# Optimization experiments

Measured on AMD Instinct MI355X. Metric: run time of the kernel, lower is better.

Reference implementation:

```python
import jax, jax.numpy as jnp
import numpy as np

B, N, D, H, L = 2, 2048, 128, 8, 3
V = 32          # NUM_ATOM_TYPES (assumed)
DH = D // H
SCALE = 1.0 / (DH ** 0.5)
NEG = -1e9      # stands in for -inf in the additive attention mask
EPS = 1e-5


def _ln(x, g, b):
    m = x.mean(-1, keepdims=True)
    v = ((x - m) ** 2).mean(-1, keepdims=True)
    return (x - m) / jnp.sqrt(v + EPS) * g + b


def setup_inputs() -> dict:
    key = jax.random.key(0)
    ks = jax.random.split(key, 24)
    nrm = lambda k, shape, std=0.02: jax.random.normal(k, shape, jnp.float32) * std
    atom_embed = nrm(ks[0], (V, D)).at[0].set(0.0)  # padding_idx = 0
    cons_embed = nrm(ks[1], (1, 1, D))
    in_w = nrm(ks[2], (D, D)); in_b = jnp.zeros((D,), jnp.float32)
    qkv_w = nrm(ks[3], (L, 3 * D, D)); qkv_b = jnp.zeros((L, 3 * D), jnp.float32)
    out_w = nrm(ks[4], (L, D, D)); out_b = jnp.zeros((L, D), jnp.float32)
    ln1_g = jnp.ones((L, D), jnp.float32); ln1_b = jnp.zeros((L, D), jnp.float32)
    ln2_g = jnp.ones((L, D), jnp.float32); ln2_b = jnp.zeros((L, D), jnp.float32)
    ff1_w = nrm(ks[5], (L, 4 * D, D)); ff1_b = jnp.zeros((L, 4 * D), jnp.float32)
    ff2_w = nrm(ks[6], (L, D, 4 * D)); ff2_b = jnp.zeros((L, D), jnp.float32)
    struct_bias = nrm(ks[7], (L,), 0.5)  # scalar per layer (init 0 in torch; randomized to exercise the path)
    head_ln_g = jnp.ones((D,), jnp.float32); head_ln_b = jnp.zeros((D,), jnp.float32)
    head_w = nrm(ks[8], (1, D)); head_b = jnp.zeros((1,), jnp.float32)
    is_atom = jax.random.bernoulli(ks[9], 0.5, (B, N))
    atom_id = jax.random.randint(ks[10], (B, N), 0, V)
    mask = jax.random.bernoulli(ks[11], 0.9, (B, N))
    adjacency = (jax.random.uniform(ks[12], (B, N, N)) < 0.002).astype(jnp.float32)
    adjacency = jnp.maximum(adjacency, jnp.eye(N, dtype=jnp.float32)[None])  # self-loops
    root_idx = jax.random.randint(ks[13], (B,), 0, N)
    return dict(atom_embed=atom_embed, cons_embed=cons_embed, in_w=in_w, in_b=in_b,
                qkv_w=qkv_w, qkv_b=qkv_b, out_w=out_w, out_b=out_b,
                ln1_g=ln1_g, ln1_b=ln1_b, ln2_g=ln2_g, ln2_b=ln2_b,
                ff1_w=ff1_w, ff1_b=ff1_b, ff2_w=ff2_w, ff2_b=ff2_b,
                struct_bias=struct_bias, head_ln_g=head_ln_g, head_ln_b=head_ln_b,
                head_w=head_w, head_b=head_b, adjacency=adjacency,
                is_atom=is_atom, atom_id=atom_id, mask=mask, root_idx=root_idx)


def reference(atom_embed, cons_embed, in_w, in_b, qkv_w, qkv_b, out_w, out_b,
              ln1_g, ln1_b, ln2_g, ln2_b, ff1_w, ff1_b, ff2_w, ff2_b,
              struct_bias, head_ln_g, head_ln_b, head_w, head_b,
              adjacency, is_atom, atom_id, mask, root_idx):
    # node embeddings
    ae = atom_embed[jnp.clip(atom_id, 0, V - 1)]                     # [B,N,D]
    h = jnp.where(is_atom[..., None], ae, jnp.broadcast_to(cons_embed, (B, N, D)))
    h = h @ in_w.T + in_b
    # additive attention mask: valid pairs OK; invalid query rows attend only to self
    pair_ok = mask[:, :, None] & mask[:, None, :]
    eye = jnp.eye(N, dtype=bool)[None]
    ok = pair_ok | ((~mask)[:, :, None] & eye)
    am = jnp.where(ok, 0.0, NEG).astype(jnp.float32)                 # [B,N,N]
    for i in range(L):
        x = _ln(h, ln1_g[i], ln1_b[i])
        qkv = (x @ qkv_w[i].T + qkv_b[i]).reshape(B, N, 3, H, DH)
        q, k, v = (jnp.transpose(qkv[:, :, j], (0, 2, 1, 3)) for j in range(3))  # [B,H,N,DH]
        scores = jnp.einsum('bhqd,bhkd->bhqk', q, k) * SCALE \
                 + struct_bias[i] * adjacency[:, None] + am[:, None]
        attn = jax.nn.softmax(scores, axis=-1)
        o = jnp.einsum('bhqk,bhkd->bhqd', attn, v)
        o = jnp.transpose(o, (0, 2, 1, 3)).reshape(B, N, D)
        h = h + (o @ out_w[i].T + out_b[i])
        x2 = _ln(h, ln2_g[i], ln2_b[i])
        f = jax.nn.gelu(x2 @ ff1_w[i].T + ff1_b[i], approximate=False)
        h = h + (f @ ff2_w[i].T + ff2_b[i])
    pooled = h[jnp.arange(B), root_idx]                              # [B,D]
    p = _ln(pooled, head_ln_g, head_ln_b)
    return (p @ head_w.T + head_b)[:, 0]                             # [B]
```

## Files before the change

kernel.cpp:

```cpp
#include <hip/hip_runtime.h>
#include <cmath>

#define NB 2
#define NN 2048
#define ND 128
#define NH 8
#define NL 3
#define NV 32
#define NDH 16
#define LN_EPS 1e-5f
#define QSCALE 0.36067376022224085f

typedef __bf16 bf8_t __attribute__((ext_vector_type(8)));
typedef __bf16 bf4_t __attribute__((ext_vector_type(4)));
typedef float f4x __attribute__((ext_vector_type(4)));
typedef float f16x __attribute__((ext_vector_type(16)));

struct CastArgs {
  const float* s[5];
  __bf16* d[5];
  int startblk[5];
};
__global__ __launch_bounds__(256) void castall_kernel(CastArgs a) {
  int blk = blockIdx.x;
  int seg = 0;
#pragma unroll
  for (int i = 1; i < 5; i++) seg += (blk >= a.startblk[i]) ? 1 : 0;
  int i4 = (blk - a.startblk[seg]) * 256 + threadIdx.x;
  float4 v = ((const float4*)a.s[seg])[i4];
  bf4_t p = {(__bf16)v.x, (__bf16)v.y, (__bf16)v.z, (__bf16)v.w};
  ((bf4_t*)a.d[seg])[i4] = p;
}

__global__ __launch_bounds__(256) void adjbits_kernel(const float* __restrict__ adj,
                                                      unsigned long long* __restrict__ bits) {
  int g = (blockIdx.x * 4 + (threadIdx.x >> 6)) * 4;
  int lane = threadIdx.x & 63;
  const float* p = adj + (size_t)g * 64 + lane;
  unsigned long long w0 = __ballot(p[0] != 0.0f);
  unsigned long long w1 = __ballot(p[64] != 0.0f);
  unsigned long long w2 = __ballot(p[128] != 0.0f);
  unsigned long long w3 = __ballot(p[192] != 0.0f);
  if (lane == 0) {
    bits[g] = w0; bits[g + 1] = w1; bits[g + 2] = w2; bits[g + 3] = w3;
  }
}

__global__ void maskbits_kernel(const int* __restrict__ mask,
                                unsigned long long* __restrict__ bits) {
  int g = blockIdx.x * 4 + (threadIdx.x >> 6);
  int lane = threadIdx.x & 63;
  int v = mask[g * 64 + lane];
  unsigned long long bal = __ballot(v != 0);
  if (lane == 0) bits[g] = bal;
}

template <int IN, int OUT2>
__global__ __launch_bounds__(512) void fused_kernel(
    const __bf16* __restrict__ Xb,
    const float* __restrict__ atom_embed, const float* __restrict__ cons_embed,
    const int* __restrict__ is_atom, const int* __restrict__ atom_id,
    const __bf16* __restrict__ W1, const float* __restrict__ b1,
    float* __restrict__ H,
    const float* __restrict__ lng, const float* __restrict__ lnb,
    const __bf16* __restrict__ W2, const float* __restrict__ b2,
    __bf16* __restrict__ Fb,
    __bf16* __restrict__ Qb, __bf16* __restrict__ Kb, __bf16* __restrict__ Vt) {
  constexpr int K1 = (IN == 2) ? 512 : 128;
  constexpr int XD = K1 + 16;
  __shared__ __bf16 Xs[16][XD];
  __shared__ __bf16 Ws[128][136];
  __shared__ float Hs[16][132];
  __shared__ __bf16 X2[16][136];
  int m0 = blockIdx.x * 16;
  int t = threadIdx.x;
  int lane = t & 63, w = t >> 6;
  int l15 = lane & 15, quad = lane >> 4;

  if constexpr (IN == 0) {
    int r = t >> 5, c = t & 31;
    int row = m0 + r;
    int id = atom_id[row];
    id = id < 0 ? 0 : (id > NV - 1 ? NV - 1 : id);
    const float* src = is_atom[row] ? (atom_embed + (size_t)id * ND) : cons_embed;
    float4 v = *(const float4*)&src[c * 4];
    bf4_t p = {(__bf16)v.x, (__bf16)v.y, (__bf16)v.z, (__bf16)v.w};
    *(bf4_t*)&Xs[r][c * 4] = p;
  } else if constexpr (IN == 1) {
    int r = t >> 5, c = t & 31;
    *(bf4_t*)&Xs[r][c * 4] = *(const bf4_t*)&Xb[(size_t)(m0 + r) * 128 + c * 4];
  } else {
#pragma unroll
    for (int c = t; c < 1024; c += 512) {
      int r = c >> 6, ch = c & 63;
      *(bf8_t*)&Xs[r][ch * 8] = *(const bf8_t*)&Xb[(size_t)(m0 + r) * 512 + ch * 8];
    }
  }

  f4x acc = {0.f, 0.f, 0.f, 0.f};
  for (int kc = 0; kc < K1 / 128; kc++) {
    if (kc) __syncthreads();
#pragma unroll
    for (int c = t; c < 2048; c += 512) {
      int r = c >> 4, ch = c & 15;
      *(bf8_t*)&Ws[r][ch * 8] = *(const bf8_t*)&W1[(size_t)r * K1 + kc * 128 + ch * 8];
    }
    __syncthreads();
#pragma unroll
    for (int kk = 0; kk < 4; kk++) {
      bf8_t a = *(const bf8_t*)&Xs[l15][kc * 128 + kk * 32 + quad * 8];
      bf8_t b = *(const bf8_t*)&Ws[w * 16 + l15][kk * 32 + quad * 8];
      acc = __builtin_amdgcn_mfma_f32_16x16x32_bf16(a, b, acc, 0, 0, 0);
    }
  }
  {
    int n = w * 16 + l15;
    float bv = b1[n];
#pragma unroll
    for (int r = 0; r < 4; r++) {
      int m = quad * 4 + r;
      float v = acc[r] + bv;
      if constexpr (IN != 0) v += H[(size_t)(m0 + m) * ND + n];
      H[(size_t)(m0 + m) * ND + n] = v;
      Hs[m][n] = v;
    }
  }
  __syncthreads();

  if constexpr (OUT2 != 0) {
    {
      int r = t >> 5, c = t & 31;
      float4 v = *(const float4*)&Hs[r][c * 4];
      float s1 = v.x + v.y + v.z + v.w;
      float s2 = v.x * v.x + v.y * v.y + v.z * v.z + v.w * v.w;
#pragma unroll
      for (int m = 16; m >= 1; m >>= 1) {
        s1 += __shfl_xor(s1, m, 64);
        s2 += __shfl_xor(s2, m, 64);
      }
      float mean = s1 * (1.0f / ND);
      float var = s2 * (1.0f / ND) - mean * mean;
      float rstd = rsqrtf(var + LN_EPS);
      float4 gg = *(const float4*)&lng[c * 4];
      float4 bb = *(const float4*)&lnb[c * 4];
      bf4_t p;
      p[0] = (__bf16)((v.x - mean) * rstd * gg.x + bb.x);
      p[1] = (__bf16)((v.y - mean) * rstd * gg.y + bb.y);
      p[2] = (__bf16)((v.z - mean) * rstd * gg.z + bb.z);
      p[3] = (__bf16)((v.w - mean) * rstd * gg.w + bb.w);
      *(bf4_t*)&X2[r][c * 4] = p;
    }
    __syncthreads();

    constexpr int NCH = (OUT2 == 1) ? 4 : 3;
#pragma unroll
    for (int nc = 0; nc < NCH; nc++) {
#pragma unroll
      for (int c = t; c < 2048; c += 512) {
        int r = c >> 4, ch = c & 15;
        *(bf8_t*)&Ws[r][ch * 8] = *(const bf8_t*)&W2[(size_t)(nc * 128 + r) * 128 + ch * 8];
      }
      __syncthreads();
      f4x a2 = {0.f, 0.f, 0.f, 0.f};
#pragma unroll
      for (int kk = 0; kk < 4; kk++) {
        bf8_t a = *(const bf8_t*)&X2[l15][kk * 32 + quad * 8];
        bf8_t b = *(const bf8_t*)&Ws[w * 16 + l15][kk * 32 + quad * 8];
        a2 = __builtin_amdgcn_mfma_f32_16x16x32_bf16(a, b, a2, 0, 0, 0);
      }
      int n = nc * 128 + w * 16 + l15;
      float bv = b2[n];
#pragma unroll
      for (int r = 0; r < 4; r++) {
        int m = m0 + quad * 4 + r;
        float v = a2[r] + bv;
        if constexpr (OUT2 == 1) {
          v = 0.5f * v * (1.0f + erff(v * 0.70710678118f));
          Fb[(size_t)m * 512 + n] = (__bf16)v;
        } else {
          if (nc == 0) Qb[(size_t)m * ND + n] = (__bf16)(v * QSCALE);
          else if (nc == 1) Kb[(size_t)m * ND + n - ND] = (__bf16)v;
          else {
            int c2 = n - 2 * ND, hh = c2 >> 4, d0 = c2 & 15;
            int bb = m >> 11, nn = m & 2047;
            Vt[((size_t)((bb * NH + hh) * NDH + d0)) * NN + nn] = (__bf16)v;
          }
        }
      }
      __syncthreads();
    }
  }
}

__global__ __launch_bounds__(512) void attn_kernel(
    const __bf16* __restrict__ Qb, const __bf16* __restrict__ Kb,
    const __bf16* __restrict__ Vt, const unsigned int* __restrict__ adjbits,
    const unsigned int* __restrict__ maskbits, const int* __restrict__ mask,
    const float* __restrict__ sbias, int layer, __bf16* __restrict__ o) {
  int b = blockIdx.z, hh = blockIdx.y, q0 = blockIdx.x * 32;
  int wave = threadIdx.x >> 6;
  int lane = threadIdx.x & 63;
  int l31 = lane & 31, hi = lane >> 5;
  int l15 = lane & 15, quad = lane >> 4;
  float esb = __expf(sbias[layer]);
  const int bN = b * NN;
  const int kw0 = wave * 256;

  __shared__ __bf16 Pbuf[8][32][40];
  __shared__ float Ored[8][32][17];
  __shared__ float Lred[8][32];

  bf8_t Qf = *(const bf8_t*)(Qb + (size_t)(bN + q0 + l31) * ND + hh * NDH + hi * 8);

  int q = q0 + l31;
  int mq = mask[bN + q];
  const unsigned int* adjp = adjbits + (size_t)(bN + q) * (NN / 32) + (kw0 >> 5);
  const unsigned int* mbp = maskbits + (bN + kw0) / 32;
  const __bf16* kp = Kb + (size_t)(bN + kw0 + l31) * ND + hh * NDH + hi * 8;
  const __bf16* vp = Vt + (size_t)((b * NH + hh) * NDH + l15) * NN + kw0 + quad * 8;

  int dq = q - kw0;
  int tsel = dq >> 5;
  unsigned int selfw = 1u << (dq & 31);
  int sh4 = hi * 4;

  f4x Olo = {0.f, 0.f, 0.f, 0.f}, Ohi = {0.f, 0.f, 0.f, 0.f};
  float ls = 0.f;

  bf8_t Kf = *(const bf8_t*)kp;
  bf8_t Vf = *(const bf8_t*)vp;
  unsigned int aw = adjp[0];
  unsigned int mkw = mbp[0];

  for (int t = 0; t < 8; t++) {
    bf8_t Kn = Kf, Vn = Vf;
    unsigned int awn = aw, mkn = mkw;
    if (t < 7) {
      kp += 32 * ND;
      Kn = *(const bf8_t*)kp;
      Vn = *(const bf8_t*)(vp + (t + 1) * 32);
      awn = adjp[t + 1];
      mkn = mbp[t + 1];
    }
    f16x S = {0.f, 0.f, 0.f, 0.f, 0.f, 0.f, 0.f, 0.f,
              0.f, 0.f, 0.f, 0.f, 0.f, 0.f, 0.f, 0.f};
    S = __builtin_amdgcn_mfma_f32_32x32x16_bf16(Kf, Qf, S, 0, 0, 0);
    unsigned int okw = mq ? mkw : ((t == tsel) ? selfw : 0u);
    unsigned int wa = (aw & okw) >> sh4;
    unsigned int okh = okw >> sh4;
#pragma unroll
    for (int g = 0; g < 4; g++) {
      bf4_t pk;
#pragma unroll
      for (int r = 0; r < 4; r++) {
        int c = g * 8 + r;
        float e = __builtin_amdgcn_exp2f(S[g * 4 + r]);
        float wgt = ((wa >> c) & 1) ? esb : (((okh >> c) & 1) ? 1.0f : 0.0f);
        float p = e * wgt;
        ls += p;
        pk[r] = (__bf16)p;
      }
      *(bf4_t*)&Pbuf[wave][l31][sh4 + g * 8] = pk;
    }
    asm volatile("s_waitcnt lgkmcnt(0)" ::: "memory");
    bf8_t Plo = *(const bf8_t*)&Pbuf[wave][l15][quad * 8];
    bf8_t Phi = *(const bf8_t*)&Pbuf[wave][16 + l15][quad * 8];
    Olo = __builtin_amdgcn_mfma_f32_16x16x32_bf16(Plo, Vf, Olo, 0, 0, 0);
    Ohi = __builtin_amdgcn_mfma_f32_16x16x32_bf16(Phi, Vf, Ohi, 0, 0, 0);
    Kf = Kn; Vf = Vn; aw = awn; mkw = mkn;
  }

  ls += __shfl_xor(ls, 32, 64);
  if (hi == 0) Lred[wave][l31] = ls;
#pragma unroll
  for (int r = 0; r < 4; r++) {
    Ored[wave][quad * 4 + r][l15] = Olo[r];
    Ored[wave][16 + quad * 4 + r][l15] = Ohi[r];
  }
  __syncthreads();
  int row = threadIdx.x >> 4, col = threadIdx.x & 15;
  float s = 0.f, L = 0.f;
#pragma unroll
  for (int p = 0; p < 8; p++) {
    s += Ored[p][row][col];
    L += Lred[p][row];
  }
  o[(size_t)(bN + q0 + row) * ND + hh * NDH + col] = (__bf16)(s / L);
}

__global__ void head_kernel(const float* __restrict__ h, const int* __restrict__ root_idx,
                            const float* __restrict__ g, const float* __restrict__ bt,
                            const float* __restrict__ hw, const float* __restrict__ hb,
                            float* __restrict__ out) {
  int b = blockIdx.x, lane = threadIdx.x;
  const float* row = h + ((size_t)b * NN + root_idx[b]) * ND;
  float2 v = *(const float2*)&row[lane * 2];
  float s1 = v.x + v.y, s2 = v.x * v.x + v.y * v.y;
#pragma unroll
  for (int m = 32; m >= 1; m >>= 1) {
    s1 += __shfl_xor(s1, m, 64);
    s2 += __shfl_xor(s2, m, 64);
  }
  float mean = s1 * (1.0f / ND);
  float var = s2 * (1.0f / ND) - mean * mean;
  float rstd = rsqrtf(var + LN_EPS);
  float p0 = (v.x - mean) * rstd * g[lane * 2] + bt[lane * 2];
  float p1 = (v.y - mean) * rstd * g[lane * 2 + 1] + bt[lane * 2 + 1];
  float part = p0 * hw[lane * 2] + p1 * hw[lane * 2 + 1];
#pragma unroll
  for (int m = 32; m >= 1; m >>= 1) part += __shfl_xor(part, m, 64);
  if (lane == 0) out[b] = part + hb[0];
}

extern "C" void kernel_launch(void* const* d_in, const int* in_sizes, int n_in,
                              void* d_out, int out_size, void* d_ws, size_t ws_size,
                              hipStream_t stream) {
  const float* atom_embed = (const float*)d_in[0];
  const float* cons_embed = (const float*)d_in[1];
  const float* in_w  = (const float*)d_in[2];
  const float* in_b  = (const float*)d_in[3];
  const float* qkv_w = (const float*)d_in[4];
  const float* qkv_b = (const float*)d_in[5];
  const float* out_w = (const float*)d_in[6];
  const float* out_b = (const float*)d_in[7];
  const float* ln1_g = (const float*)d_in[8];
  const float* ln1_b = (const float*)d_in[9];
  const float* ln2_g = (const float*)d_in[10];
  const float* ln2_b = (const float*)d_in[11];
  const float* ff1_w = (const float*)d_in[12];
  const float* ff1_b = (const float*)d_in[13];
  const float* ff2_w = (const float*)d_in[14];
  const float* ff2_b = (const float*)d_in[15];
  const float* sbias = (const float*)d_in[16];
  const float* hg    = (const float*)d_in[17];
  const float* hbt   = (const float*)d_in[18];
  const float* hw    = (const float*)d_in[19];
  const float* hb    = (const float*)d_in[20];
  const float* adj   = (const float*)d_in[21];
  const int* is_atom = (const int*)d_in[22];
  const int* atom_id = (const int*)d_in[23];
  const int* mask    = (const int*)d_in[24];
  const int* root_idx= (const int*)d_in[25];
  float* out = (float*)d_out;

  const int MR = NB * NN;
  float* h = (float*)d_ws;
  __bf16* ob   = (__bf16*)(h + MR * ND);
  __bf16* fb   = ob + MR * ND;
  __bf16* Qb   = fb + MR * 512;
  __bf16* Kb   = Qb + MR * ND;
  __bf16* Vt   = Kb + MR * ND;
  __bf16* wbin = Vt + MR * ND;
  __bf16* wbqkv= wbin + ND * ND;
  __bf16* wbout= wbqkv + NL * 384 * ND;
  __bf16* wbff1= wbout + NL * ND * ND;
  __bf16* wbff2= wbff1 + NL * 512 * ND;
  unsigned int* adjb = (unsigned int*)(wbff2 + NL * ND * 512);
  unsigned int* mskb = adjb + NB * NN * NN / 32;

  CastArgs ca;
  ca.s[0] = in_w;  ca.d[0] = wbin;  ca.startblk[0] = 0;
  ca.s[1] = qkv_w; ca.d[1] = wbqkv; ca.startblk[1] = 16;
  ca.s[2] = out_w; ca.d[2] = wbout; ca.startblk[2] = 160;
  ca.s[3] = ff1_w; ca.d[3] = wbff1; ca.startblk[3] = 208;
  ca.s[4] = ff2_w; ca.d[4] = wbff2; ca.startblk[4] = 400;
  castall_kernel<<<592, 256, 0, stream>>>(ca);
  adjbits_kernel<<<NB * NN * NN / 64 / 16, 256, 0, stream>>>(adj, (unsigned long long*)adjb);
  maskbits_kernel<<<16, 256, 0, stream>>>(mask, (unsigned long long*)mskb);

  fused_kernel<0, 2><<<MR / 16, 512, 0, stream>>>(
      nullptr, atom_embed, cons_embed, is_atom, atom_id,
      wbin, in_b, h, ln1_g, ln1_b,
      wbqkv, qkv_b, nullptr, Qb, Kb, Vt);

  for (int i = 0; i < NL; i++) {
    attn_kernel<<<dim3(NN / 32, NH, NB), 512, 0, stream>>>(
        Qb, Kb, Vt, adjb, mskb, mask, sbias, i, ob);
    fused_kernel<1, 1><<<MR / 16, 512, 0, stream>>>(
        ob, nullptr, nullptr, nullptr, nullptr,
        wbout + (size_t)i * ND * ND, out_b + i * ND, h,
        ln2_g + i * ND, ln2_b + i * ND,
        wbff1 + (size_t)i * 512 * ND, ff1_b + i * 512, fb,
        nullptr, nullptr, nullptr);
    if (i < NL - 1) {
      fused_kernel<2, 2><<<MR / 16, 512, 0, stream>>>(
          fb, nullptr, nullptr, nullptr, nullptr,
          wbff2 + (size_t)i * ND * 512, ff2_b + i * ND, h,
          ln1_g + (i + 1) * ND, ln1_b + (i + 1) * ND,
          wbqkv + (size_t)(i + 1) * 384 * ND, qkv_b + (i + 1) * 384, nullptr,
          Qb, Kb, Vt);
    } else {
      fused_kernel<2, 0><<<MR / 16, 512, 0, stream>>>(
          fb, nullptr, nullptr, nullptr, nullptr,
          wbff2 + (size_t)i * ND * 512, ff2_b + i * ND, h,
          nullptr, nullptr, nullptr, nullptr, nullptr,
          nullptr, nullptr, nullptr);
    }
  }
  head_kernel<<<NB, 64, 0, stream>>>(h, root_idx, hg, hbt, hw, hb, out);
}
```

Before: 280.3 us.

## Split fused GEMM blocks across output chunks, prefetch weights, merge prep and head kernels

Merges the cast, adjacency-bit and mask-bit kernels into one prep launch, and folds the head into the last fused kernel. Fused kernels now use a second grid dimension that splits the second GEMM's output chunks across two blocks. Each block recomputes the first GEMM, and the residual stream is ping-ponged between two buffers so the duplicate blocks don't race. Weight tiles are prefetched into registers one stage ahead to overlap global loads with MFMA, at the cost of redundant first-GEMM work and more register pressure.

```diff
diff --git a/kernel.cpp b/kernel.cpp
--- a/kernel.cpp
+++ b/kernel.cpp
@@ -21,38 +21,35 @@
   __bf16* d[5];
   int startblk[5];
 };
-__global__ __launch_bounds__(256) void castall_kernel(CastArgs a) {
+__global__ __launch_bounds__(256) void prep_kernel(
+    CastArgs a, const float* __restrict__ adj, unsigned long long* __restrict__ abits,
+    const int* __restrict__ mask, unsigned long long* __restrict__ mbits) {
   int blk = blockIdx.x;
-  int seg = 0;
-#pragma unroll
-  for (int i = 1; i < 5; i++) seg += (blk >= a.startblk[i]) ? 1 : 0;
-  int i4 = (blk - a.startblk[seg]) * 256 + threadIdx.x;
-  float4 v = ((const float4*)a.s[seg])[i4];
-  bf4_t p = {(__bf16)v.x, (__bf16)v.y, (__bf16)v.z, (__bf16)v.w};
-  ((bf4_t*)a.d[seg])[i4] = p;
-}
-
-__global__ __launch_bounds__(256) void adjbits_kernel(const float* __restrict__ adj,
-                                                      unsigned long long* __restrict__ bits) {
-  int g = (blockIdx.x * 4 + (threadIdx.x >> 6)) * 4;
   int lane = threadIdx.x & 63;
-  const float* p = adj + (size_t)g * 64 + lane;
-  unsigned long long w0 = __ballot(p[0] != 0.0f);
-  unsigned long long w1 = __ballot(p[64] != 0.0f);
-  unsigned long long w2 = __ballot(p[128] != 0.0f);
-  unsigned long long w3 = __ballot(p[192] != 0.0f);
-  if (lane == 0) {
-    bits[g] = w0; bits[g + 1] = w1; bits[g + 2] = w2; bits[g + 3] = w3;
-  }
-}
-
-__global__ void maskbits_kernel(const int* __restrict__ mask,
-                                unsigned long long* __restrict__ bits) {
-  int g = blockIdx.x * 4 + (threadIdx.x >> 6);
-  int lane = threadIdx.x & 63;
-  int v = mask[g * 64 + lane];
-  unsigned long long bal = __ballot(v != 0);
-  if (lane == 0) bits[g] = bal;
+  if (blk < 592) {
+    int seg = 0;
+#pragma unroll
+    for (int i = 1; i < 5; i++) seg += (blk >= a.startblk[i]) ? 1 : 0;
+    int i4 = (blk - a.startblk[seg]) * 256 + threadIdx.x;
+    float4 v = ((const float4*)a.s[seg])[i4];
+    bf4_t p = {(__bf16)v.x, (__bf16)v.y, (__bf16)v.z, (__bf16)v.w};
+    ((bf4_t*)a.d[seg])[i4] = p;
+  } else if (blk < 592 + 8192) {
+    int g = ((blk - 592) * 4 + (threadIdx.x >> 6)) * 4;
+    const float* p = adj + (size_t)g * 64 + lane;
+    unsigned long long w0 = __ballot(p[0] != 0.0f);
+    unsigned long long w1 = __ballot(p[64] != 0.0f);
+    unsigned long long w2 = __ballot(p[128] != 0.0f);
+    unsigned long long w3 = __ballot(p[192] != 0.0f);
+    if (lane == 0) {
+      abits[g] = w0; abits[g + 1] = w1; abits[g + 2] = w2; abits[g + 3] = w3;
+    }
+  } else {
+    int g = (blk - 8784) * 4 + (threadIdx.x >> 6);
+    int v = mask[g * 64 + lane];
+    unsigned long long bal = __ballot(v != 0);
+    if (lane == 0) mbits[g] = bal;
+  }
 }
 
 template <int IN, int OUT2>
@@ -61,21 +58,27 @@
     const float* __restrict__ atom_embed, const float* __restrict__ cons_embed,
     const int* __restrict__ is_atom, const int* __restrict__ atom_id,
     const __bf16* __restrict__ W1, const float* __restrict__ b1,
-    float* __restrict__ H,
+    const float* __restrict__ Hin, float* __restrict__ Hout,
     const float* __restrict__ lng, const float* __restrict__ lnb,
     const __bf16* __restrict__ W2, const float* __restrict__ b2,
     __bf16* __restrict__ Fb,
-    __bf16* __restrict__ Qb, __bf16* __restrict__ Kb, __bf16* __restrict__ Vt) {
+    __bf16* __restrict__ Qb, __bf16* __restrict__ Kb, __bf16* __restrict__ Vt,
+    const int* __restrict__ root_idx, const float* __restrict__ hg,
+    const float* __restrict__ hbt, const float* __restrict__ hwp,
+    const float* __restrict__ hbp, float* __restrict__ outp) {
   constexpr int K1 = (IN == 2) ? 512 : 128;
-  constexpr int XD = K1 + 16;
-  __shared__ __bf16 Xs[16][XD];
+  constexpr int NK1 = K1 / 128;
+  __shared__ __bf16 Xs[16][K1 + 8];
   __shared__ __bf16 Ws[128][136];
   __shared__ float Hs[16][132];
   __shared__ __bf16 X2[16][136];
   int m0 = blockIdx.x * 16;
+  int g = blockIdx.y;
   int t = threadIdx.x;
   int lane = t & 63, w = t >> 6;
   int l15 = lane & 15, quad = lane >> 4;
+  const int NC2 = (OUT2 == 1) ? 2 : (OUT2 == 2 ? (g == 0 ? 2 : 1) : 0);
+  const int T = NK1 + NC2;
 
   if constexpr (IN == 0) {
     int r = t >> 5, c = t & 31;
@@ -97,70 +100,81 @@
     }
   }
 
+  bf8_t wreg[4];
+  auto issue = [&](int i) {
+    const __bf16* base;
+    int stride, rowoff, coloff;
+    if (i < NK1) {
+      base = W1; stride = K1; rowoff = 0; coloff = i * 128;
+    } else {
+      int j = i - NK1;
+      int nc = (OUT2 == 1) ? (2 * g + j) : (g == 0 ? j : 2);
+      base = W2; stride = 128; rowoff = nc * 128; coloff = 0;
+    }
+#pragma unroll
+    for (int jj = 0; jj < 4; jj++) {
+      int c = t + jj * 512;
+      int r = c >> 4, ch = c & 15;
+      wreg[jj] = *(const bf8_t*)&base[(size_t)(rowoff + r) * stride + coloff + ch * 8];
+    }
+  };
+  issue(0);
+
   f4x acc = {0.f, 0.f, 0.f, 0.f};
-  for (int kc = 0; kc < K1 / 128; kc++) {
-    if (kc) __syncthreads();
-#pragma unroll
-    for (int c = t; c < 2048; c += 512) {
-      int r = c >> 4, ch = c & 15;
-      *(bf8_t*)&Ws[r][ch * 8] = *(const bf8_t*)&W1[(size_t)r * K1 + kc * 128 + ch * 8];
+  for (int i = 0; i < T; i++) {
+    if (i) __syncthreads();
+#pragma unroll
+    for (int jj = 0; jj < 4; jj++) {
+      int c = t + jj * 512;
+      *(bf8_t*)&Ws[c >> 4][(c & 15) * 8] = wreg[jj];
     }
     __syncthreads();
-#pragma unroll
-    for (int kk = 0; kk < 4; kk++) {
-      bf8_t a = *(const bf8_t*)&Xs[l15][kc * 128 + kk * 32 + quad * 8];
-      bf8_t b = *(const bf8_t*)&Ws[w * 16 + l15][kk * 32 + quad * 8];
-      acc = __builtin_amdgcn_mfma_f32_16x16x32_bf16(a, b, acc, 0, 0, 0);
-    }
-  }
-  {
-    int n = w * 16 + l15;
-    float bv = b1[n];
-#pragma unroll
-    for (int r = 0; r < 4; r++) {
-      int m = quad * 4 + r;
-      float v = acc[r] + bv;
-      if constexpr (IN != 0) v += H[(size_t)(m0 + m) * ND + n];
-      H[(size_t)(m0 + m) * ND + n] = v;
-      Hs[m][n] = v;
-    }
-  }
-  __syncthreads();
-
-  if constexpr (OUT2 != 0) {
-    {
-      int r = t >> 5, c = t & 31;
-      float4 v = *(const float4*)&Hs[r][c * 4];
-      float s1 = v.x + v.y + v.z + v.w;
-      float s2 = v.x * v.x + v.y * v.y + v.z * v.z + v.w * v.w;
-#pragma unroll
-      for (int m = 16; m >= 1; m >>= 1) {
-        s1 += __shfl_xor(s1, m, 64);
-        s2 += __shfl_xor(s2, m, 64);
-      }
-      float mean = s1 * (1.0f / ND);
-      float var = s2 * (1.0f / ND) - mean * mean;
-      float rstd = rsqrtf(var + LN_EPS);
-      float4 gg = *(const float4*)&lng[c * 4];
-      float4 bb = *(const float4*)&lnb[c * 4];
-      bf4_t p;
-      p[0] = (__bf16)((v.x - mean) * rstd * gg.x + bb.x);
-      p[1] = (__bf16)((v.y - mean) * rstd * gg.y + bb.y);
-      p[2] = (__bf16)((v.z - mean) * rstd * gg.z + bb.z);
-      p[3] = (__bf16)((v.w - mean) * rstd * gg.w + bb.w);
-      *(bf4_t*)&X2[r][c * 4] = p;
-    }
-    __syncthreads();
-
-    constexpr int NCH = (OUT2 == 1) ? 4 : 3;
-#pragma unroll
-    for (int nc = 0; nc < NCH; nc++) {
-#pragma unroll
-      for (int c = t; c < 2048; c += 512) {
-        int r = c >> 4, ch = c & 15;
-        *(bf8_t*)&Ws[r][ch * 8] = *(const bf8_t*)&W2[(size_t)(nc * 128 + r) * 128 + ch * 8];
-      }
-      __syncthreads();
+    if (i + 1 < T) issue(i + 1);
+    if (i < NK1) {
+#pragma unroll
+      for (int kk = 0; kk < 4; kk++) {
+        bf8_t a = *(const bf8_t*)&Xs[l15][i * 128 + kk * 32 + quad * 8];
+        bf8_t b = *(const bf8_t*)&Ws[w * 16 + l15][kk * 32 + quad * 8];
+        acc = __builtin_amdgcn_mfma_f32_16x16x32_bf16(a, b, acc, 0, 0, 0);
+      }
+      if (i == NK1 - 1) {
+        int n = w * 16 + l15;
+        float bv = b1[n];
+#pragma unroll
+        for (int r = 0; r < 4; r++) {
+          int m = quad * 4 + r;
+          float v = acc[r] + bv;
+          if constexpr (IN != 0) v += Hin[(size_t)(m0 + m) * ND + n];
+          if (g == 0) Hout[(size_t)(m0 + m) * ND + n] = v;
+          Hs[m][n] = v;
+        }
+        __syncthreads();
+        if constexpr (OUT2 != 0) {
+          int r = t >> 5, c = t & 31;
+          float4 v = *(const float4*)&Hs[r][c * 4];
+          float s1 = v.x + v.y + v.z + v.w;
+          float s2 = v.x * v.x + v.y * v.y + v.z * v.z + v.w * v.w;
+#pragma unroll
+          for (int m = 16; m >= 1; m >>= 1) {
+            s1 += __shfl_xor(s1, m, 64);
+            s2 += __shfl_xor(s2, m, 64);
+          }
+          float mean = s1 * (1.0f / ND);
+          float var = s2 * (1.0f / ND) - mean * mean;
+          float rstd = rsqrtf(var + LN_EPS);
+          float4 gg = *(const float4*)&lng[c * 4];
+          float4 bb = *(const float4*)&lnb[c * 4];
+          bf4_t p;
+          p[0] = (__bf16)((v.x - mean) * rstd * gg.x + bb.x);
+          p[1] = (__bf16)((v.y - mean) * rstd * gg.y + bb.y);
+          p[2] = (__bf16)((v.z - mean) * rstd * gg.z + bb.z);
+          p[3] = (__bf16)((v.w - mean) * rstd * gg.w + bb.w);
+          *(bf4_t*)&X2[r][c * 4] = p;
+        }
+      }
+    } else {
+      int j = i - NK1;
+      int nc = (OUT2 == 1) ? (2 * g + j) : (g == 0 ? j : 2);
       f4x a2 = {0.f, 0.f, 0.f, 0.f};
 #pragma unroll
       for (int kk = 0; kk < 4; kk++) {
@@ -178,16 +192,41 @@
           v = 0.5f * v * (1.0f + erff(v * 0.70710678118f));
           Fb[(size_t)m * 512 + n] = (__bf16)v;
         } else {
-          if (nc == 0) Qb[(size_t)m * ND + n] = (__bf16)(v * QSCALE);
-          else if (nc == 1) Kb[(size_t)m * ND + n - ND] = (__bf16)v;
+          if (n < ND) Qb[(size_t)m * ND + n] = (__bf16)(v * QSCALE);
+          else if (n < 2 * ND) Kb[(size_t)m * ND + n - ND] = (__bf16)v;
           else {
             int c2 = n - 2 * ND, hh = c2 >> 4, d0 = c2 & 15;
-            int bb = m >> 11, nn = m & 2047;
-            Vt[((size_t)((bb * NH + hh) * NDH + d0)) * NN + nn] = (__bf16)v;
+            int bb2 = m >> 11, nn = m & 2047;
+            Vt[((size_t)((bb2 * NH + hh) * NDH + d0)) * NN + nn] = (__bf16)v;
           }
         }
       }
-      __syncthreads();
+    }
+  }
+
+  if constexpr (OUT2 == 0) {
+    if (w < NB) {
+      int rt = root_idx[w];
+      int rglob = w * NN + rt;
+      if (rglob >= m0 && rglob < m0 + 16) {
+        int r = rglob - m0;
+        float v0 = Hs[r][2 * lane], v1 = Hs[r][2 * lane + 1];
+        float s1 = v0 + v1, s2 = v0 * v0 + v1 * v1;
+#pragma unroll
+        for (int m = 32; m >= 1; m >>= 1) {
+          s1 += __shfl_xor(s1, m, 64);
+          s2 += __shfl_xor(s2, m, 64);
+        }
+        float mean = s1 * (1.0f / ND);
+        float var = s2 * (1.0f / ND) - mean * mean;
+        float rstd = rsqrtf(var + LN_EPS);
+        float p0 = (v0 - mean) * rstd * hg[2 * lane] + hbt[2 * lane];
+        float p1 = (v1 - mean) * rstd * hg[2 * lane + 1] + hbt[2 * lane + 1];
+        float part = p0 * hwp[2 * lane] + p1 * hwp[2 * lane + 1];
+#pragma unroll
+        for (int m = 32; m >= 1; m >>= 1) part += __shfl_xor(part, m, 64);
+        if (lane == 0) outp[w] = part + hbp[0];
+      }
     }
   }
 }
@@ -249,18 +288,18 @@
     unsigned int wa = (aw & okw) >> sh4;
     unsigned int okh = okw >> sh4;
 #pragma unroll
-    for (int g = 0; g < 4; g++) {
+    for (int gg = 0; gg < 4; gg++) {
       bf4_t pk;
 #pragma unroll
       for (int r = 0; r < 4; r++) {
-        int c = g * 8 + r;
-        float e = __builtin_amdgcn_exp2f(S[g * 4 + r]);
+        int c = gg * 8 + r;
+        float e = __builtin_amdgcn_exp2f(S[gg * 4 + r]);
         float wgt = ((wa >> c) & 1) ? esb : (((okh >> c) & 1) ? 1.0f : 0.0f);
         float p = e * wgt;
         ls += p;
         pk[r] = (__bf16)p;
       }
-      *(bf4_t*)&Pbuf[wave][l31][sh4 + g * 8] = pk;
+      *(bf4_t*)&Pbuf[wave][l31][sh4 + gg * 8] = pk;
     }
     asm volatile("s_waitcnt lgkmcnt(0)" ::: "memory");
     bf8_t Plo = *(const bf8_t*)&Pbuf[wave][l15][quad * 8];
@@ -286,30 +325,6 @@
     L += Lred[p][row];
   }
   o[(size_t)(bN + q0 + row) * ND + hh * NDH + col] = (__bf16)(s / L);
-}
-
-__global__ void head_kernel(const float* __restrict__ h, const int* __restrict__ root_idx,
-                            const float* __restrict__ g, const float* __restrict__ bt,
-                            const float* __restrict__ hw, const float* __restrict__ hb,
-                            float* __restrict__ out) {
-  int b = blockIdx.x, lane = threadIdx.x;
-  const float* row = h + ((size_t)b * NN + root_idx[b]) * ND;
-  float2 v = *(const float2*)&row[lane * 2];
-  float s1 = v.x + v.y, s2 = v.x * v.x + v.y * v.y;
-#pragma unroll
-  for (int m = 32; m >= 1; m >>= 1) {
-    s1 += __shfl_xor(s1, m, 64);
-    s2 += __shfl_xor(s2, m, 64);
-  }
-  float mean = s1 * (1.0f / ND);
-  float var = s2 * (1.0f / ND) - mean * mean;
-  float rstd = rsqrtf(var + LN_EPS);
-  float p0 = (v.x - mean) * rstd * g[lane * 2] + bt[lane * 2];
-  float p1 = (v.y - mean) * rstd * g[lane * 2 + 1] + bt[lane * 2 + 1];
-  float part = p0 * hw[lane * 2] + p1 * hw[lane * 2 + 1];
-#pragma unroll
-  for (int m = 32; m >= 1; m >>= 1) part += __shfl_xor(part, m, 64);
-  if (lane == 0) out[b] = part + hb[0];
 }
 
 extern "C" void kernel_launch(void* const* d_in, const int* in_sizes, int n_in,
@@ -344,9 +359,9 @@
   float* out = (float*)d_out;
 
   const int MR = NB * NN;
-  float* h = (float*)d_ws;
-  __bf16* ob   = (__bf16*)(h + MR * ND);
-  __bf16* fb   = ob + MR * ND;
+  float* hA = (float*)d_ws;
+  float* hB = hA + MR * ND;
+  __bf16* fb   = (__bf16*)(hB + MR * ND);
   __bf16* Qb   = fb + MR * 512;
   __bf16* Kb   = Qb + MR * ND;
   __bf16* Vt   = Kb + MR * ND;
@@ -357,6 +372,7 @@
   __bf16* wbff2= wbff1 + NL * 512 * ND;
   unsigned int* adjb = (unsigned int*)(wbff2 + NL * ND * 512);
   unsigned int* mskb = adjb + NB * NN * NN / 32;
+  __bf16* ob = (__bf16*)(mskb + 128);
 
   CastArgs ca;
   ca.s[0] = in_w;  ca.d[0] = wbin;  ca.startblk[0] = 0;
@@ -364,38 +380,40 @@
   ca.s[2] = out_w; ca.d[2] = wbout; ca.startblk[2] = 160;
   ca.s[3] = ff1_w; ca.d[3] = wbff1; ca.startblk[3] = 208;
   ca.s[4] = ff2_w; ca.d[4] = wbff2; ca.startblk[4] = 400;
-  castall_kernel<<<592, 256, 0, stream>>>(ca);
-  adjbits_kernel<<<NB * NN * NN / 64 / 16, 256, 0, stream>>>(adj, (unsigned long long*)adjb);
-  maskbits_kernel<<<16, 256, 0, stream>>>(mask, (unsigned long long*)mskb);
-
-  fused_kernel<0, 2><<<MR / 16, 512, 0, stream>>>(
+  prep_kernel<<<8800, 256, 0, stream>>>(ca, adj, (unsigned long long*)adjb,
+                                        mask, (unsigned long long*)mskb);
+
+  fused_kernel<0, 2><<<dim3(MR / 16, 2), 512, 0, stream>>>(
       nullptr, atom_embed, cons_embed, is_atom, atom_id,
-      wbin, in_b, h, ln1_g, ln1_b,
-      wbqkv, qkv_b, nullptr, Qb, Kb, Vt);
+      wbin, in_b, nullptr, hA, ln1_g, ln1_b,
+      wbqkv, qkv_b, nullptr, Qb, Kb, Vt,
+      nullptr, nullptr, nullptr, nullptr, nullptr, nullptr);
 
   for (int i = 0; i < NL; i++) {
     attn_kernel<<<dim3(NN / 32, NH, NB), 512, 0, stream>>>(
         Qb, Kb, Vt, adjb, mskb, mask, sbias, i, ob);
-    fused_kernel<1, 1><<<MR / 16, 512, 0, stream>>>(
+    fused_kernel<1, 1><<<dim3(MR / 16, 2), 512, 0, stream>>>(
         ob, nullptr, nullptr, nullptr, nullptr,
-        wbout + (size_t)i * ND * ND, out_b + i * ND, h,
+        wbout + (size_t)i * ND * ND, out_b + i * ND, hA, hB,
         ln2_g + i * ND, ln2_b + i * ND,
         wbff1 + (size_t)i * 512 * ND, ff1_b + i * 512, fb,
-        nullptr, nullptr, nullptr);
+        nullptr, nullptr, nullptr,
+        nullptr, nullptr, nullptr, nullptr, nullptr, nullptr);
     if (i < NL - 1) {
-      fused_kernel<2, 2><<<MR / 16, 512, 0, stream>>>(
+      fused_kernel<2, 2><<<dim3(MR / 16, 2), 512, 0, stream>>>(
           fb, nullptr, nullptr, nullptr, nullptr,
-          wbff2 + (size_t)i * ND * 512, ff2_b + i * ND, h,
+          wbff2 + (size_t)i * ND * 512, ff2_b + i * ND, hB, hA,
           ln1_g + (i + 1) * ND, ln1_b + (i + 1) * ND,
           wbqkv + (size_t)(i + 1) * 384 * ND, qkv_b + (i + 1) * 384, nullptr,
-          Qb, Kb, Vt);
+          Qb, Kb, Vt,
+          nullptr, nullptr, nullptr, nullptr, nullptr, nullptr);
     } else {
-      fused_kernel<2, 0><<<MR / 16, 512, 0, stream>>>(
+      fused_kernel<2, 0><<<dim3(MR / 16, 1), 512, 0, stream>>>(
           fb, nullptr, nullptr, nullptr, nullptr,
-          wbff2 + (size_t)i * ND * 512, ff2_b + i * ND, h,
+          wbff2 + (size_t)i * ND * 512, ff2_b + i * ND, hB, hA,
           nullptr, nullptr, nullptr, nullptr, nullptr,
-          nullptr, nullptr, nullptr);
-    }
-  }
-  head_kernel<<<NB, 64, 0, stream>>>(h, root_idx, hg, hbt, hw, hb, out);
+          nullptr, nullptr, nullptr,
+          root_idx, hg, hbt, hw, hb, out);
+    }
+  }
 }
```

After: 264.8 us. 5.5% less time.
